# Kernel optimization log

Measured on AMD Instinct MI355X. Metric: run time of the kernel, lower is better.

The kernel has to match this reference:

```python
import jax, jax.numpy as jnp
import numpy as np
import math

N = 4096
E = 131072
D_IN = 148      # d_node_feat
D_HID = 128     # d_node_reshape (DIHGNN.d_node_feat)
D_OUT = 148     # d_output


def setup_inputs() -> dict:
    key = jax.random.key(0)
    ks = jax.random.split(key, 10)
    node_feat = jax.random.normal(ks[0], (1, N, D_IN), dtype=jnp.float32)
    edge_index = jax.random.randint(ks[1], (2, E), 0, N, dtype=jnp.int64)
    # learned parameters
    W1 = jax.random.normal(ks[2], (D_HID, D_IN), dtype=jnp.float32) * 0.02
    b1 = jnp.zeros((D_HID,), dtype=jnp.float32)
    a_param = jnp.array([0.9], dtype=jnp.float32)   # DIHGNN.a
    Wd = jax.random.normal(ks[3], (D_OUT, D_HID), dtype=jnp.float32) * 0.02
    bd = jnp.zeros((D_OUT,), dtype=jnp.float32)
    W2 = jax.random.normal(ks[4], (2, D_OUT), dtype=jnp.float32) * 0.02
    b2 = jnp.zeros((2,), dtype=jnp.float32)
    return {"node_feat": node_feat, "edge_index": edge_index, "num_node": N,
            "W1": W1, "b1": b1, "a_param": a_param, "Wd": Wd, "bd": bd,
            "W2": W2, "b2": b2}


def reference(node_feat, edge_index, num_node, W1, b1, a_param, Wd, bd, W2, b2):
    n = num_node
    x = node_feat[0]                                   # [N, D_IN]
    x = x @ W1.T + b1                                  # linear_1 -> [N, D_HID]

    # dense adjacency via scatter-set (duplicates collapse to 1, as in torch)
    adj = jnp.zeros((n, n), dtype=jnp.float32).at[edge_index[0], edge_index[1]].set(1.0)

    # asymmetric degree normalization: D_col^{-1/2} A D_row^{-1/2}
    L = adj.sum(axis=0)                                # column sums
    R = adj.sum(axis=1)                                # row sums
    L_is = jnp.where(L > 0, jax.lax.rsqrt(jnp.maximum(L, 1e-30)), 0.0)
    R_is = jnp.where(R > 0, jax.lax.rsqrt(jnp.maximum(R, 1e-30)), 0.0)
    adj_norm = L_is[:, None] * adj * R_is[None, :]

    # custom tanh: 0.5 + 0.5 * tanh(2 * a)
    alpha = 0.5 + 0.5 * jnp.tanh(2.0 * a_param[0])     # scalar

    # graph diffusion: (I - alpha * A_norm)^{-1} x, as a linear solve
    eye = jnp.eye(n, dtype=jnp.float32)
    x = jnp.linalg.solve(eye - alpha * adj_norm, x)    # [N, D_HID]

    x = x @ Wd.T + bd                                  # DIHGNN.linear -> [N, D_OUT]

    # similarity loss (scaled by DIHGNN.d_node_feat = D_HID)
    sim = (x @ x.T) / math.sqrt(D_HID)                 # [N, N]
    sim = sim * (1.0 - eye)                            # zero diagonal
    sim = jax.nn.relu(sim)
    loss = sim.sum() / (n * (n - 1))

    x = x * (1.0 - alpha)
    x = jax.nn.relu(x)
    pooled = jnp.max(x, axis=0, keepdims=True)         # global_max_pool, single graph -> [1, D_OUT]
    out = pooled @ W2.T + b2                           # [1, 2]
    return (out, loss)
```

## Files before the change

### kernel.cpp

```cpp
#include <hip/hip_runtime.h>
#include <hip/hip_bf16.h>
#include <math.h>

#define N_NODES 4096
#define N_EDGES 131072
#define BCAP 80
#define DIN 148
#define DHID 128
#define DOUT 148
#define KP 160
#define NITER 6

typedef __attribute__((ext_vector_type(8))) _Float16 half8;
typedef __attribute__((ext_vector_type(4))) float f32x4;

__device__ inline float h2f(unsigned e) {
    union { unsigned short u; _Float16 h; } cv;
    cv.u = (unsigned short)(e & 0xffffu);
    return (float)cv.h;
}

__global__ __launch_bounds__(256) void prep_kernel(const int* __restrict__ ei,
                                                   const float* __restrict__ W1,
                                                   const float* __restrict__ Wd,
                                                   float* __restrict__ W1T,
                                                   float* __restrict__ WdT,
                                                   unsigned* __restrict__ bitmap,
                                                   unsigned* __restrict__ bucket,
                                                   int* __restrict__ rowdeg,
                                                   int* __restrict__ coldeg) {
    int gtid = blockIdx.x * 256 + threadIdx.x;
    if (gtid < DIN * DHID) {
        int kk = gtid >> 7, d = gtid & 127;
        W1T[gtid] = W1[d * DIN + kk];
    } else if (gtid < DIN * DHID + DHID * DOUT) {
        int i2 = gtid - DIN * DHID;
        int h = i2 / DOUT, o = i2 - h * DOUT;
        WdT[i2] = Wd[o * DHID + h];
    }
    int i = ei[gtid] & (N_NODES - 1);
    int j = ei[gtid + N_EDGES] & (N_NODES - 1);
    unsigned pos = (unsigned)i * (unsigned)N_NODES + (unsigned)j;
    unsigned w = pos >> 5, m = 1u << (pos & 31u);
    unsigned old = atomicOr(&bitmap[w], m);
    if (!(old & m)) {
        int p = atomicAdd(&rowdeg[i], 1);
        if (p < BCAP) bucket[i * BCAP + p] = (unsigned)j;
        atomicAdd(&coldeg[j], 1);
    }
}

__global__ __launch_bounds__(256) void finalize_kernel(unsigned* __restrict__ bucket,
                                                       const int* __restrict__ rowdeg,
                                                       const int* __restrict__ coldeg,
                                                       float* __restrict__ acoef,
                                                       const float* __restrict__ a_param,
                                                       const float* __restrict__ nf,
                                                       const float* __restrict__ W1T,
                                                       const float* __restrict__ b1,
                                                       float* __restrict__ Bm) {
    int tid = threadIdx.x, bid = blockIdx.x;
    int r0 = bid * 8;
    for (int idx = tid; idx < 8 * BCAP; idx += 256) {
        int r = r0 + idx / BCAP, q = idx % BCAP;
        int dg = min(rowdeg[r], BCAP);
        if (q < dg) {
            unsigned col = bucket[r * BCAP + q];
            int rd = rowdeg[col];
            float rsj = (rd > 0) ? rsqrtf((float)rd) : 0.0f;
            union { _Float16 h; unsigned short u; } cv;
            cv.h = (_Float16)rsj;
            bucket[r * BCAP + q] = (col << 16) | (unsigned)cv.u;
        }
    }
    if (tid < 8) {
        int r = r0 + tid;
        float alpha = 0.5f + 0.5f * tanhf(2.0f * a_param[0]);
        int cd = coldeg[r];
        acoef[r] = (cd > 0) ? alpha * rsqrtf((float)cd) : 0.0f;
    }
    __shared__ float sA[8 * 152];
    for (int idx = tid; idx < 8 * DIN; idx += 256) {
        int nd = idx / DIN, c = idx - nd * DIN;
        sA[nd * 152 + c] = nf[(r0 + nd) * DIN + c];
    }
    __syncthreads();
    int half = tid >> 7, d = tid & 127;
    float a0 = 0.f, a1 = 0.f, a2 = 0.f, a3 = 0.f;
    const float* sb8 = sA + half * 4 * 152;
    for (int kk = 0; kk < DIN; ++kk) {
        float wv = W1T[kk * DHID + d];
        a0 += sb8[0 * 152 + kk] * wv;
        a1 += sb8[1 * 152 + kk] * wv;
        a2 += sb8[2 * 152 + kk] * wv;
        a3 += sb8[3 * 152 + kk] * wv;
    }
    float bb = b1[d];
    int node0 = r0 + half * 4;
    Bm[(node0 + 0) * DHID + d] = a0 + bb;
    Bm[(node0 + 1) * DHID + d] = a1 + bb;
    Bm[(node0 + 2) * DHID + d] = a2 + bb;
    Bm[(node0 + 3) * DHID + d] = a3 + bb;
}

template<bool LAST>
__global__ __launch_bounds__(256) void spmv_kernel(const float* __restrict__ xin,
                                                   float* __restrict__ xout,
                                                   const float* __restrict__ Bm,
                                                   const float* __restrict__ prev2,
                                                   const unsigned* __restrict__ cc,
                                                   const int* __restrict__ rowdeg,
                                                   const float* __restrict__ acoef,
                                                   double* __restrict__ accd) {
    int tid = threadIdx.x;
    int wid = __builtin_amdgcn_readfirstlane(tid >> 6);
    int lane = tid & 63;
    int r = blockIdx.x * 4 + wid;
    int dg8 = (min(rowdeg[r], BCAP) + 7) & ~7;
    int nch = dg8 >> 3;
    const uint4* __restrict__ q = (const uint4*)(cc + r * BCAP);
    const float2* __restrict__ x2 = (const float2*)xin;
    float ax = 0.f, ay = 0.f;
    uint4 qa0 = q[0], qb0 = q[1];
    float2 v0 = x2[(qa0.x >> 16) * 64 + lane];
    float2 v1 = x2[(qa0.y >> 16) * 64 + lane];
    float2 v2 = x2[(qa0.z >> 16) * 64 + lane];
    float2 v3 = x2[(qa0.w >> 16) * 64 + lane];
    float2 v4 = x2[(qb0.x >> 16) * 64 + lane];
    float2 v5 = x2[(qb0.y >> 16) * 64 + lane];
    float2 v6 = x2[(qb0.z >> 16) * 64 + lane];
    float2 v7 = x2[(qb0.w >> 16) * 64 + lane];
    uint4 qa1 = q[2], qb1 = q[3];
    for (int c = 0; c < nch; ++c) {
        float2 w0 = x2[(qa1.x >> 16) * 64 + lane];
        float2 w1 = x2[(qa1.y >> 16) * 64 + lane];
        float2 w2 = x2[(qa1.z >> 16) * 64 + lane];
        float2 w3 = x2[(qa1.w >> 16) * 64 + lane];
        float2 w4 = x2[(qb1.x >> 16) * 64 + lane];
        float2 w5 = x2[(qb1.y >> 16) * 64 + lane];
        float2 w6 = x2[(qb1.z >> 16) * 64 + lane];
        float2 w7 = x2[(qb1.w >> 16) * 64 + lane];
        uint4 na = q[2 * c + 4], nb = q[2 * c + 5];
        float c0 = h2f(qa0.x), c1 = h2f(qa0.y), c2f = h2f(qa0.z), c3 = h2f(qa0.w);
        float c4 = h2f(qb0.x), c5 = h2f(qb0.y), c6 = h2f(qb0.z), c7 = h2f(qb0.w);
        ax += c0 * v0.x + c1 * v1.x + c2f * v2.x + c3 * v3.x
            + c4 * v4.x + c5 * v5.x + c6 * v6.x + c7 * v7.x;
        ay += c0 * v0.y + c1 * v1.y + c2f * v2.y + c3 * v3.y
            + c4 * v4.y + c5 * v5.y + c6 * v6.y + c7 * v7.y;
        qa0 = qa1; qb0 = qb1; qa1 = na; qb1 = nb;
        v0 = w0; v1 = w1; v2 = w2; v3 = w3;
        v4 = w4; v5 = w5; v6 = w6; v7 = w7;
    }
    float ac = acoef[r];
    int idx = r * 64 + lane;
    float2 b = ((const float2*)Bm)[idx];
    float vx = b.x + ac * ax, vy = b.y + ac * ay;
    ((float2*)xout)[idx] = make_float2(vx, vy);
    if (LAST) {
        float2 xp = ((const float2*)xin)[idx];
        float2 p2 = ((const float2*)prev2)[idx];
        float dpx = xp.x - p2.x, dpy = xp.y - p2.y;
        float dnx = vx - xp.x, dny = vy - xp.y;
        double s0 = (double)dpx * dpx + (double)dpy * dpy;
        double s1 = (double)dnx * dpx + (double)dny * dpy;
        __shared__ double sh0[256], sh1[256];
        sh0[tid] = s0; sh1[tid] = s1;
        __syncthreads();
        for (int off = 128; off > 0; off >>= 1) {
            if (tid < off) { sh0[tid] += sh0[tid + off]; sh1[tid] += sh1[tid + off]; }
            __syncthreads();
        }
        if (tid == 0) { atomicAdd(&accd[1], sh0[0]); atomicAdd(&accd[2], sh1[0]); }
    }
}

__global__ __launch_bounds__(256) void post_kernel(const float* __restrict__ last,
                                                   const float* __restrict__ prev,
                                                   const double* __restrict__ accd,
                                                   const float* __restrict__ WdT,
                                                   const float* __restrict__ bd,
                                                   _Float16* __restrict__ yH,
                                                   unsigned* __restrict__ mcolu) {
    int tid = threadIdx.x, bid = blockIdx.x;
    double d0 = accd[1], d1 = accd[2];
    float lam = (d0 > 0.0) ? (float)(d1 / d0) : 0.0f;
    float den = 1.0f - lam;
    if (fabsf(den) < 1e-4f) den = (den < 0.0f) ? -1e-4f : 1e-4f;
    float sf = fminf(fmaxf(lam / den, -1e4f), 1e4f);
    __shared__ float sx[8 * DHID];
    for (int idx = tid; idx < 8 * DHID; idx += 256) {
        int node = bid * 8 + (idx >> 7), ccol = idx & 127;
        float l = last[node * DHID + ccol];
        sx[idx] = l + sf * (l - prev[node * DHID + ccol]);
    }
    __syncthreads();
    if (tid < DOUT) {
        float acc[8];
#pragma unroll
        for (int nd = 0; nd < 8; ++nd) acc[nd] = 0.f;
        for (int h = 0; h < DHID; ++h) {
            float wv = WdT[h * DOUT + tid];
#pragma unroll
            for (int nd = 0; nd < 8; ++nd) acc[nd] += sx[nd * DHID + h] * wv;
        }
        float bb = bd[tid];
        float lm = 0.0f;
#pragma unroll
        for (int nd = 0; nd < 8; ++nd) {
            int node = bid * 8 + nd;
            float v = acc[nd] + bb;
            yH[node * KP + tid] = (_Float16)v;
            lm = fmaxf(lm, v);
        }
        atomicMax(&mcolu[tid], __float_as_uint(lm));
    } else {
        int i2 = tid - DOUT;
        if (i2 < 8 * (KP - DOUT)) {
            int node = bid * 8 + i2 / (KP - DOUT);
            int ccol = DOUT + i2 % (KP - DOUT);
            yH[node * KP + ccol] = (_Float16)0.0f;
        }
    }
}

__global__ __launch_bounds__(256) void simloss_kernel(const _Float16* __restrict__ yH,
                                                      double* __restrict__ accd,
                                                      unsigned* __restrict__ cnt,
                                                      const unsigned* __restrict__ mcolu,
                                                      const float* __restrict__ W2,
                                                      const float* __restrict__ b2,
                                                      const float* __restrict__ a_param,
                                                      float* __restrict__ out) {
    int tid = threadIdx.x;
    int tb = blockIdx.x;
    int ti = 0, rem = tb;
    while (rem >= 32 - ti) { rem -= 32 - ti; ++ti; }
    int tj = ti + rem;
    int wid = tid >> 6, lane = tid & 63;
    int wr = wid >> 1, wc = wid & 1;
    int fr = lane & 15, kq = lane >> 4;
    const half8* __restrict__ ap =
        (const half8*)(yH + (size_t)(ti * 128 + wr * 64 + fr) * KP);
    const half8* __restrict__ bp =
        (const half8*)(yH + (size_t)(tj * 128 + wc * 64 + fr) * KP);
    f32x4 C[4][4];
#pragma unroll
    for (int m = 0; m < 4; ++m)
#pragma unroll
        for (int n = 0; n < 4; ++n) C[m][n] = (f32x4)0.0f;
#pragma unroll
    for (int kk = 0; kk < KP / 32; ++kk) {
        half8 a[4], bf[4];
#pragma unroll
        for (int m = 0; m < 4; ++m) a[m] = ap[m * 320 + kk * 4 + kq];
#pragma unroll
        for (int n = 0; n < 4; ++n) bf[n] = bp[n * 320 + kk * 4 + kq];
#pragma unroll
        for (int m = 0; m < 4; ++m)
#pragma unroll
            for (int n = 0; n < 4; ++n)
                C[m][n] = __builtin_amdgcn_mfma_f32_16x16x32_f16(a[m], bf[n], C[m][n], 0, 0, 0);
    }
    const float inv = 0.0883883476483184405f;
    float wgt = (ti == tj) ? 1.0f : 2.0f;
    float lsum = 0.0f;
    int rq = kq * 4;
#pragma unroll
    for (int m = 0; m < 4; ++m)
#pragma unroll
        for (int n = 0; n < 4; ++n)
#pragma unroll
            for (int reg = 0; reg < 4; ++reg) {
                int gi = ti * 128 + wr * 64 + m * 16 + rq + reg;
                int gj = tj * 128 + wc * 64 + n * 16 + fr;
                float v = C[m][n][reg] * inv;
                if (gi != gj && v > 0.0f) lsum += wgt * v;
            }
    for (int o2 = 32; o2 > 0; o2 >>= 1) lsum += __shfl_down(lsum, o2);
    __shared__ float ws[4];
    __shared__ bool lastblk;
    if ((tid & 63) == 0) ws[tid >> 6] = lsum;
    __syncthreads();
    if (tid == 0) {
        atomicAdd(&accd[0], (double)(ws[0] + ws[1] + ws[2] + ws[3]));
        __threadfence();
        unsigned r = __hip_atomic_fetch_add(&cnt[1], 1u, __ATOMIC_ACQ_REL,
                                            __HIP_MEMORY_SCOPE_AGENT);
        lastblk = (r == 527u);
    }
    __syncthreads();
    if (lastblk && tid < 64) {
        float alpha = 0.5f + 0.5f * tanhf(2.0f * a_param[0]);
        float oma = 1.0f - alpha;
        float s0 = 0.0f, s1 = 0.0f;
        for (int o = tid; o < DOUT; o += 64) {
            float p = __uint_as_float(mcolu[o]);
            s0 += p * W2[o];
            s1 += p * W2[DOUT + o];
        }
        for (int off = 32; off > 0; off >>= 1) {
            s0 += __shfl_down(s0, off);
            s1 += __shfl_down(s1, off);
        }
        if (tid == 0) {
            double loss = __hip_atomic_load(&accd[0], __ATOMIC_RELAXED,
                                            __HIP_MEMORY_SCOPE_AGENT);
            out[0] = b2[0] + oma * s0;
            out[1] = b2[1] + oma * s1;
            out[2] = (float)(loss / (4096.0 * 4095.0));
        }
    }
}

extern "C" void kernel_launch(void* const* d_in, const int* in_sizes, int n_in,
                              void* d_out, int out_size, void* d_ws, size_t ws_size,
                              hipStream_t stream) {
    (void)in_sizes; (void)n_in; (void)out_size; (void)ws_size;
    const float* node_feat  = (const float*)d_in[0];
    const int*   edge_index = (const int*)d_in[1];
    const float* W1         = (const float*)d_in[3];
    const float* b1         = (const float*)d_in[4];
    const float* a_param    = (const float*)d_in[5];
    const float* Wd         = (const float*)d_in[6];
    const float* bd         = (const float*)d_in[7];
    const float* W2         = (const float*)d_in[8];
    const float* b2         = (const float*)d_in[9];
    float*       out        = (float*)d_out;

    char* w = (char*)d_ws;
    size_t off = 0;
    auto alloc = [&](size_t bytes) -> char* {
        char* p = w + off;
        off = (off + bytes + 255) & ~(size_t)255;
        return p;
    };
    double*   accd    = (double*)   alloc(8 * sizeof(double));
    unsigned* cnt     = (unsigned*) alloc(16 * sizeof(unsigned));
    int*      rowdeg  = (int*)      alloc(N_NODES * 4);
    int*      coldeg  = (int*)      alloc(N_NODES * 4);
    unsigned* mcolu   = (unsigned*) alloc(256 * 4);
    unsigned* bitmap  = (unsigned*) alloc((size_t)N_NODES * N_NODES / 8);
    unsigned* bucket  = (unsigned*) alloc((size_t)N_NODES * BCAP * 4 + 1024);
    size_t zero_end = off;
    float*    acoef   = (float*)    alloc(N_NODES * 4);
    float*    W1T     = (float*)    alloc(DIN * DHID * 4);
    float*    WdT     = (float*)    alloc(DHID * DOUT * 4);
    float*    Bm      = (float*)    alloc(N_NODES * DHID * 4);
    float*    Y0      = (float*)    alloc(N_NODES * DHID * 4);
    float*    Y1      = (float*)    alloc(N_NODES * DHID * 4);
    float*    Y2      = (float*)    alloc(N_NODES * DHID * 4);
    _Float16* yH      = (_Float16*) alloc((size_t)N_NODES * KP * 2);

    hipMemsetAsync(w, 0, zero_end, stream);

    prep_kernel<<<N_EDGES / 256, 256, 0, stream>>>(edge_index, W1, Wd, W1T, WdT,
                                                   bitmap, bucket, rowdeg, coldeg);
    finalize_kernel<<<N_NODES / 8, 256, 0, stream>>>(bucket, rowdeg, coldeg, acoef,
                                                     a_param, node_feat, W1T, b1, Bm);

    float* rot[3] = {Y0, Y1, Y2};
    const float* cur = Bm;
    for (int it = 0; it < NITER - 1; ++it) {
        float* dst = rot[it % 3];
        spmv_kernel<false><<<N_NODES / 4, 256, 0, stream>>>(cur, dst, Bm, nullptr, bucket,
                                                            rowdeg, acoef, accd);
        cur = dst;
    }
    float* lastb = rot[(NITER - 1) % 3];
    float* prevb = rot[(NITER - 2) % 3];
    float* prev2 = rot[(NITER - 3) % 3];
    spmv_kernel<true><<<N_NODES / 4, 256, 0, stream>>>(cur, lastb, Bm, prev2, bucket,
                                                       rowdeg, acoef, accd);

    post_kernel<<<N_NODES / 8, 256, 0, stream>>>(lastb, prevb, accd, WdT, bd, yH, mcolu);
    simloss_kernel<<<528, 256, 0, stream>>>(yH, accd, cnt, mcolu, W2, b2, a_param, out);
}
```

Measured before the change: 167.6 us.

## Store early diffusion iterates in fp16 and double rows per finalize/post block

The first four SpMV iterations now gather from and write packed fp16 iterates, halving the bytes of the random neighbour gathers. The last iterations stay in fp32 so the extrapolation step still sees full-precision differences. Finalize now also emits an fp16 copy of the bias term. Finalize and post kernels handle 16 rows per block instead of 8 for more reuse of the weight loads. The fp16 iterates add rounding error to the early diffusion steps.

Result: faster. 157.3 us (-6.1%).

```diff
diff --git a/kernel.cpp b/kernel.cpp
--- a/kernel.cpp
+++ b/kernel.cpp
@@ -18,6 +18,15 @@
     union { unsigned short u; _Float16 h; } cv;
     cv.u = (unsigned short)(e & 0xffffu);
     return (float)cv.h;
+}
+__device__ inline float2 h2f2(unsigned p) {
+    union { unsigned u; _Float16 h[2]; } cv; cv.u = p;
+    return make_float2((float)cv.h[0], (float)cv.h[1]);
+}
+__device__ inline unsigned f2h2(float x, float y) {
+    union { unsigned u; _Float16 h[2]; } cv;
+    cv.h[0] = (_Float16)x; cv.h[1] = (_Float16)y;
+    return cv.u;
 }
 
 __global__ __launch_bounds__(256) void prep_kernel(const int* __restrict__ ei,
@@ -58,10 +67,11 @@
                                                        const float* __restrict__ nf,
                                                        const float* __restrict__ W1T,
                                                        const float* __restrict__ b1,
-                                                       float* __restrict__ Bm) {
+                                                       float* __restrict__ Bm,
+                                                       unsigned* __restrict__ Bh) {
     int tid = threadIdx.x, bid = blockIdx.x;
-    int r0 = bid * 8;
-    for (int idx = tid; idx < 8 * BCAP; idx += 256) {
+    int r0 = bid * 16;
+    for (int idx = tid; idx < 16 * BCAP; idx += 256) {
         int r = r0 + idx / BCAP, q = idx % BCAP;
         int dg = min(rowdeg[r], BCAP);
         if (q < dg) {
@@ -73,39 +83,47 @@
             bucket[r * BCAP + q] = (col << 16) | (unsigned)cv.u;
         }
     }
-    if (tid < 8) {
+    if (tid < 16) {
         int r = r0 + tid;
         float alpha = 0.5f + 0.5f * tanhf(2.0f * a_param[0]);
         int cd = coldeg[r];
         acoef[r] = (cd > 0) ? alpha * rsqrtf((float)cd) : 0.0f;
     }
-    __shared__ float sA[8 * 152];
-    for (int idx = tid; idx < 8 * DIN; idx += 256) {
+    __shared__ float sA[16 * 152];
+    __shared__ float sB[16 * 128];
+    for (int idx = tid; idx < 16 * DIN; idx += 256) {
         int nd = idx / DIN, c = idx - nd * DIN;
         sA[nd * 152 + c] = nf[(r0 + nd) * DIN + c];
     }
     __syncthreads();
     int half = tid >> 7, d = tid & 127;
-    float a0 = 0.f, a1 = 0.f, a2 = 0.f, a3 = 0.f;
-    const float* sb8 = sA + half * 4 * 152;
+    float a[8];
+#pragma unroll
+    for (int n = 0; n < 8; ++n) a[n] = 0.f;
+    const float* sb8 = sA + half * 8 * 152;
     for (int kk = 0; kk < DIN; ++kk) {
         float wv = W1T[kk * DHID + d];
-        a0 += sb8[0 * 152 + kk] * wv;
-        a1 += sb8[1 * 152 + kk] * wv;
-        a2 += sb8[2 * 152 + kk] * wv;
-        a3 += sb8[3 * 152 + kk] * wv;
+#pragma unroll
+        for (int n = 0; n < 8; ++n) a[n] += sb8[n * 152 + kk] * wv;
     }
     float bb = b1[d];
-    int node0 = r0 + half * 4;
-    Bm[(node0 + 0) * DHID + d] = a0 + bb;
-    Bm[(node0 + 1) * DHID + d] = a1 + bb;
-    Bm[(node0 + 2) * DHID + d] = a2 + bb;
-    Bm[(node0 + 3) * DHID + d] = a3 + bb;
-}
-
-template<bool LAST>
-__global__ __launch_bounds__(256) void spmv_kernel(const float* __restrict__ xin,
-                                                   float* __restrict__ xout,
+#pragma unroll
+    for (int n = 0; n < 8; ++n) {
+        int nd = half * 8 + n;
+        float v = a[n] + bb;
+        Bm[(r0 + nd) * DHID + d] = v;
+        sB[nd * 128 + d] = v;
+    }
+    __syncthreads();
+    for (int idx = tid; idx < 16 * 64; idx += 256) {
+        int nd = idx >> 6, dp = idx & 63;
+        Bh[(r0 + nd) * 64 + dp] = f2h2(sB[nd * 128 + 2 * dp], sB[nd * 128 + 2 * dp + 1]);
+    }
+}
+
+template<bool INH, bool OUTH, bool LAST>
+__global__ __launch_bounds__(256) void spmv_kernel(const void* __restrict__ xin_,
+                                                   void* __restrict__ xout_,
                                                    const float* __restrict__ Bm,
                                                    const float* __restrict__ prev2,
                                                    const unsigned* __restrict__ cc,
@@ -119,27 +137,21 @@
     int dg8 = (min(rowdeg[r], BCAP) + 7) & ~7;
     int nch = dg8 >> 3;
     const uint4* __restrict__ q = (const uint4*)(cc + r * BCAP);
-    const float2* __restrict__ x2 = (const float2*)xin;
+    const unsigned* __restrict__ xh = (const unsigned*)xin_;
+    const float2* __restrict__ x2 = (const float2*)xin_;
+    auto ldx = [&](unsigned e) -> float2 {
+        int col = (int)(e >> 16);
+        if constexpr (INH) return h2f2(xh[col * 64 + lane]);
+        else return x2[col * 64 + lane];
+    };
     float ax = 0.f, ay = 0.f;
     uint4 qa0 = q[0], qb0 = q[1];
-    float2 v0 = x2[(qa0.x >> 16) * 64 + lane];
-    float2 v1 = x2[(qa0.y >> 16) * 64 + lane];
-    float2 v2 = x2[(qa0.z >> 16) * 64 + lane];
-    float2 v3 = x2[(qa0.w >> 16) * 64 + lane];
-    float2 v4 = x2[(qb0.x >> 16) * 64 + lane];
-    float2 v5 = x2[(qb0.y >> 16) * 64 + lane];
-    float2 v6 = x2[(qb0.z >> 16) * 64 + lane];
-    float2 v7 = x2[(qb0.w >> 16) * 64 + lane];
+    float2 v0 = ldx(qa0.x), v1 = ldx(qa0.y), v2 = ldx(qa0.z), v3 = ldx(qa0.w);
+    float2 v4 = ldx(qb0.x), v5 = ldx(qb0.y), v6 = ldx(qb0.z), v7 = ldx(qb0.w);
     uint4 qa1 = q[2], qb1 = q[3];
     for (int c = 0; c < nch; ++c) {
-        float2 w0 = x2[(qa1.x >> 16) * 64 + lane];
-        float2 w1 = x2[(qa1.y >> 16) * 64 + lane];
-        float2 w2 = x2[(qa1.z >> 16) * 64 + lane];
-        float2 w3 = x2[(qa1.w >> 16) * 64 + lane];
-        float2 w4 = x2[(qb1.x >> 16) * 64 + lane];
-        float2 w5 = x2[(qb1.y >> 16) * 64 + lane];
-        float2 w6 = x2[(qb1.z >> 16) * 64 + lane];
-        float2 w7 = x2[(qb1.w >> 16) * 64 + lane];
+        float2 w0 = ldx(qa1.x), w1 = ldx(qa1.y), w2 = ldx(qa1.z), w3 = ldx(qa1.w);
+        float2 w4 = ldx(qb1.x), w5 = ldx(qb1.y), w6 = ldx(qb1.z), w7 = ldx(qb1.w);
         uint4 na = q[2 * c + 4], nb = q[2 * c + 5];
         float c0 = h2f(qa0.x), c1 = h2f(qa0.y), c2f = h2f(qa0.z), c3 = h2f(qa0.w);
         float c4 = h2f(qb0.x), c5 = h2f(qb0.y), c6 = h2f(qb0.z), c7 = h2f(qb0.w);
@@ -155,9 +167,13 @@
     int idx = r * 64 + lane;
     float2 b = ((const float2*)Bm)[idx];
     float vx = b.x + ac * ax, vy = b.y + ac * ay;
-    ((float2*)xout)[idx] = make_float2(vx, vy);
-    if (LAST) {
-        float2 xp = ((const float2*)xin)[idx];
+    if constexpr (OUTH) {
+        ((unsigned*)xout_)[idx] = f2h2(vx, vy);
+    } else {
+        ((float2*)xout_)[idx] = make_float2(vx, vy);
+    }
+    if constexpr (LAST) {
+        float2 xp = ((const float2*)xin_)[idx];
         float2 p2 = ((const float2*)prev2)[idx];
         float dpx = xp.x - p2.x, dpy = xp.y - p2.y;
         float dnx = vx - xp.x, dny = vy - xp.y;
@@ -182,44 +198,42 @@
                                                    _Float16* __restrict__ yH,
                                                    unsigned* __restrict__ mcolu) {
     int tid = threadIdx.x, bid = blockIdx.x;
+    int r0 = bid * 16;
     double d0 = accd[1], d1 = accd[2];
     float lam = (d0 > 0.0) ? (float)(d1 / d0) : 0.0f;
     float den = 1.0f - lam;
     if (fabsf(den) < 1e-4f) den = (den < 0.0f) ? -1e-4f : 1e-4f;
     float sf = fminf(fmaxf(lam / den, -1e4f), 1e4f);
-    __shared__ float sx[8 * DHID];
-    for (int idx = tid; idx < 8 * DHID; idx += 256) {
-        int node = bid * 8 + (idx >> 7), ccol = idx & 127;
+    __shared__ float sx[16 * DHID];
+    for (int idx = tid; idx < 16 * DHID; idx += 256) {
+        int node = r0 + (idx >> 7), ccol = idx & 127;
         float l = last[node * DHID + ccol];
         sx[idx] = l + sf * (l - prev[node * DHID + ccol]);
     }
     __syncthreads();
+    for (int idx = tid; idx < 16 * (KP - DOUT); idx += 256) {
+        int node = r0 + idx / (KP - DOUT);
+        int ccol = DOUT + idx % (KP - DOUT);
+        yH[node * KP + ccol] = (_Float16)0.0f;
+    }
     if (tid < DOUT) {
-        float acc[8];
-#pragma unroll
-        for (int nd = 0; nd < 8; ++nd) acc[nd] = 0.f;
+        float acc[16];
+#pragma unroll
+        for (int nd = 0; nd < 16; ++nd) acc[nd] = 0.f;
         for (int h = 0; h < DHID; ++h) {
             float wv = WdT[h * DOUT + tid];
 #pragma unroll
-            for (int nd = 0; nd < 8; ++nd) acc[nd] += sx[nd * DHID + h] * wv;
+            for (int nd = 0; nd < 16; ++nd) acc[nd] += sx[nd * DHID + h] * wv;
         }
         float bb = bd[tid];
         float lm = 0.0f;
 #pragma unroll
-        for (int nd = 0; nd < 8; ++nd) {
-            int node = bid * 8 + nd;
+        for (int nd = 0; nd < 16; ++nd) {
             float v = acc[nd] + bb;
-            yH[node * KP + tid] = (_Float16)v;
+            yH[(r0 + nd) * KP + tid] = (_Float16)v;
             lm = fmaxf(lm, v);
         }
         atomicMax(&mcolu[tid], __float_as_uint(lm));
-    } else {
-        int i2 = tid - DOUT;
-        if (i2 < 8 * (KP - DOUT)) {
-            int node = bid * 8 + i2 / (KP - DOUT);
-            int ccol = DOUT + i2 % (KP - DOUT);
-            yH[node * KP + ccol] = (_Float16)0.0f;
-        }
     }
 }
 
@@ -346,6 +360,9 @@
     float*    W1T     = (float*)    alloc(DIN * DHID * 4);
     float*    WdT     = (float*)    alloc(DHID * DOUT * 4);
     float*    Bm      = (float*)    alloc(N_NODES * DHID * 4);
+    unsigned* Bh      = (unsigned*) alloc((size_t)N_NODES * 64 * 4);
+    unsigned* H0      = (unsigned*) alloc((size_t)N_NODES * 64 * 4);
+    unsigned* H1      = (unsigned*) alloc((size_t)N_NODES * 64 * 4);
     float*    Y0      = (float*)    alloc(N_NODES * DHID * 4);
     float*    Y1      = (float*)    alloc(N_NODES * DHID * 4);
     float*    Y2      = (float*)    alloc(N_NODES * DHID * 4);
@@ -355,23 +372,17 @@
 
     prep_kernel<<<N_EDGES / 256, 256, 0, stream>>>(edge_index, W1, Wd, W1T, WdT,
                                                    bitmap, bucket, rowdeg, coldeg);
-    finalize_kernel<<<N_NODES / 8, 256, 0, stream>>>(bucket, rowdeg, coldeg, acoef,
-                                                     a_param, node_feat, W1T, b1, Bm);
-
-    float* rot[3] = {Y0, Y1, Y2};
-    const float* cur = Bm;
-    for (int it = 0; it < NITER - 1; ++it) {
-        float* dst = rot[it % 3];
-        spmv_kernel<false><<<N_NODES / 4, 256, 0, stream>>>(cur, dst, Bm, nullptr, bucket,
-                                                            rowdeg, acoef, accd);
-        cur = dst;
-    }
-    float* lastb = rot[(NITER - 1) % 3];
-    float* prevb = rot[(NITER - 2) % 3];
-    float* prev2 = rot[(NITER - 3) % 3];
-    spmv_kernel<true><<<N_NODES / 4, 256, 0, stream>>>(cur, lastb, Bm, prev2, bucket,
-                                                       rowdeg, acoef, accd);
-
-    post_kernel<<<N_NODES / 8, 256, 0, stream>>>(lastb, prevb, accd, WdT, bd, yH, mcolu);
+    finalize_kernel<<<N_NODES / 16, 256, 0, stream>>>(bucket, rowdeg, coldeg, acoef,
+                                                      a_param, node_feat, W1T, b1, Bm, Bh);
+
+    const int GB = N_NODES / 4;
+    spmv_kernel<true,  true,  false><<<GB, 256, 0, stream>>>(Bh, H0, Bm, nullptr, bucket, rowdeg, acoef, accd);
+    spmv_kernel<true,  true,  false><<<GB, 256, 0, stream>>>(H0, H1, Bm, nullptr, bucket, rowdeg, acoef, accd);
+    spmv_kernel<true,  true,  false><<<GB, 256, 0, stream>>>(H1, H0, Bm, nullptr, bucket, rowdeg, acoef, accd);
+    spmv_kernel<true,  false, false><<<GB, 256, 0, stream>>>(H0, Y0, Bm, nullptr, bucket, rowdeg, acoef, accd);
+    spmv_kernel<false, false, false><<<GB, 256, 0, stream>>>(Y0, Y1, Bm, nullptr, bucket, rowdeg, acoef, accd);
+    spmv_kernel<false, false, true ><<<GB, 256, 0, stream>>>(Y1, Y2, Bm, Y0, bucket, rowdeg, acoef, accd);
+
+    post_kernel<<<N_NODES / 16, 256, 0, stream>>>(Y2, Y1, accd, WdT, bd, yH, mcolu);
     simloss_kernel<<<528, 256, 0, stream>>>(yH, accd, cnt, mcolu, W2, b2, a_param, out);
 }
```
